# Kernel optimization log

Measured on AMD Instinct MI355X. Metric: run time of the kernel, lower is better.

Reference implementation:

```python
import jax, jax.numpy as jnp
import numpy as np

N_RAYS = 65536
N_SAMPLES = 96


def setup_inputs() -> dict:
    key = jax.random.key(0)
    k1, k2, k3 = jax.random.split(key, 3)
    rgb = jax.random.uniform(k1, (N_RAYS, N_SAMPLES, 3), dtype=jnp.float32)
    # SDF values near the surface, small magnitude
    sdf = jax.random.normal(k2, (N_RAYS, N_SAMPLES), dtype=jnp.float32) * 0.1
    # monotonically increasing sample depths along each ray
    z_vals = jnp.sort(
        jax.random.uniform(k3, (N_RAYS, N_SAMPLES), dtype=jnp.float32,
                           minval=0.1, maxval=5.0), axis=-1)
    return {"rgb": rgb, "sdf": sdf, "z_vals": z_vals, "beta": 10}


def reference(rgb, sdf, z_vals, beta):
    # sdf2alpha: alpha = 1 - exp(-beta * sigmoid(-sdf * beta))
    alpha = 1.0 - jnp.exp(-beta * jax.nn.sigmoid(-sdf * beta))  # [N, S]
    # exclusive cumprod of (1 - alpha + 1e-10): transmittance
    trans = jnp.cumprod(
        jnp.concatenate([jnp.ones_like(alpha[:, :1]), 1.0 - alpha + 1e-10],
                        axis=-1), axis=-1)[:, :-1]  # [N, S]
    weights = alpha * trans  # [N, S]
    rendered_rgb = jnp.sum(weights[..., None] * rgb, axis=-2)  # [N, 3]
    rendered_depth = jnp.sum(weights * z_vals, axis=-1)  # [N]
    return (rendered_depth, rendered_rgb, sdf, z_vals)
```

## Files before the change

### kernel.cpp

```cpp
#include <hip/hip_runtime.h>


#define SDFR_NS 96

struct f3 { float x, y, z; };
typedef float fv4 __attribute__((ext_vector_type(4)));

__global__ __launch_bounds__(256, 8) void sdf_compute_kernel(
    const float* __restrict__ rgb,
    const float* __restrict__ sdf,
    const float* __restrict__ z_vals,
    const int*   __restrict__ beta_p,
    float* __restrict__ out_depth,
    float* __restrict__ out_rgb,
    int n_rays)
{
    const int tid = blockIdx.x * 256 + threadIdx.x;
    const int ray = tid >> 5;
    const int l   = tid & 31;
    if (ray >= n_rays) return;

    const int sb = ray * SDFR_NS + 3 * l;
    const int rb = ray * (SDFR_NS * 3) + 9 * l;

    const f3 sv = *(const f3*)(sdf    + sb);
    const f3 zv = *(const f3*)(z_vals + sb);
    const f3 ca = *(const f3*)(rgb + rb + 0);
    const f3 cb = *(const f3*)(rgb + rb + 3);
    const f3 cc = *(const f3*)(rgb + rb + 6);
    __builtin_amdgcn_sched_barrier(0);

    int bi = *beta_p;
    float beta;
    if (bi > 1000000 || bi < -1000000) {
        union { int i; float f; } u; u.i = bi; beta = u.f;
    } else {
        beta = (float)bi;
    }

    const float e0 = __expf(-beta * __builtin_amdgcn_rcpf(1.0f + __expf(sv.x * beta)));
    const float e1 = __expf(-beta * __builtin_amdgcn_rcpf(1.0f + __expf(sv.y * beta)));
    const float e2 = __expf(-beta * __builtin_amdgcn_rcpf(1.0f + __expf(sv.z * beta)));
    const float a0 = 1.0f - e0, t0 = e0 + 1e-10f;
    const float a1 = 1.0f - e1, t1 = e1 + 1e-10f;
    const float a2 = 1.0f - e2, t2 = e2 + 1e-10f;

    float scan = t0 * t1 * t2;
    #pragma unroll
    for (int d = 1; d < 32; d <<= 1) {
        float v = __shfl_up(scan, d, 32);
        if (l >= d) scan *= v;
    }
    float E = __shfl_up(scan, 1, 32);
    if (l == 0) E = 1.0f;

    const float w0 = a0 * E;
    const float w1 = a1 * E * t0;
    const float w2 = a2 * E * t0 * t1;

    float depth = w0 * zv.x + w1 * zv.y + w2 * zv.z;
    float r0    = w0 * ca.x + w1 * cb.x + w2 * cc.x;
    float r1    = w0 * ca.y + w1 * cb.y + w2 * cc.y;
    float r2    = w0 * ca.z + w1 * cb.z + w2 * cc.z;

    #pragma unroll
    for (int d = 16; d >= 1; d >>= 1) {
        depth += __shfl_xor(depth, d, 32);
        r0    += __shfl_xor(r0, d, 32);
        r1    += __shfl_xor(r1, d, 32);
        r2    += __shfl_xor(r2, d, 32);
    }

    if (l == 0) {
        out_depth[ray] = depth;
        f3 o; o.x = r0; o.y = r1; o.z = r2;
        *(f3*)(out_rgb + ray * 3) = o;
    }
}

#define SDFR_CPB 2048

__global__ __launch_bounds__(256, 8) void sdf_copy_kernel(
    const float* __restrict__ sdf,
    const float* __restrict__ z_vals,
    float* __restrict__ out_sdf,
    float* __restrict__ out_z,
    int n_rays)
{
    const int n4     = (n_rays * SDFR_NS) / 4;
    const int stride = SDFR_CPB * 256;
    const fv4* __restrict__ s4 = (const fv4*)sdf;
    const fv4* __restrict__ z4 = (const fv4*)z_vals;
    fv4* __restrict__ os4 = (fv4*)out_sdf;
    fv4* __restrict__ oz4 = (fv4*)out_z;

    for (int i = blockIdx.x * 256 + threadIdx.x; i < n4; i += stride) {
        const fv4 a = s4[i];
        const fv4 b = z4[i];
        __builtin_nontemporal_store(a, os4 + i);
        __builtin_nontemporal_store(b, oz4 + i);
    }
}

extern "C" void kernel_launch(void* const* d_in, const int* in_sizes, int n_in,
                              void* d_out, int out_size, void* d_ws, size_t ws_size,
                              hipStream_t stream) {
    (void)n_in; (void)d_ws; (void)ws_size; (void)out_size;

    const float* rgb    = (const float*)d_in[0];
    const float* sdf    = (const float*)d_in[1];
    const float* z      = (const float*)d_in[2];
    const int*   beta_p = (const int*)d_in[3];

    const int n_rays = in_sizes[1] / SDFR_NS;

    float* out_depth = (float*)d_out;
    float* out_rgb   = out_depth + n_rays;
    float* out_sdf   = out_rgb   + (size_t)n_rays * 3;
    float* out_z     = out_sdf   + (size_t)n_rays * SDFR_NS;

    const int comp_blocks = (n_rays * 32 + 255) / 256;
    sdf_compute_kernel<<<comp_blocks, 256, 0, stream>>>(
        rgb, sdf, z, beta_p, out_depth, out_rgb, n_rays);

    sdf_copy_kernel<<<SDFR_CPB, 256, 0, stream>>>(
        sdf, z, out_sdf, out_z, n_rays);
}
```

Baseline: 175.1 us.

## Stage ray inputs into LDS via direct global-to-LDS loads with XCD-aware block remap

The compute kernel now loads each block's 8 rays of sdf, z and rgb into shared memory with 16-byte global_load_lds transfers instead of uncoalesced 12-byte per-lane vector loads. Lanes then read their three samples from LDS. Block indices are also remapped so that consecutive blocks land on the same XCD, which is meant to improve L2 locality. This adds a barrier and LDS traffic, and the remap assumes the grid size is divisible by 8.

```diff
diff --git a/kernel.cpp b/kernel.cpp
--- a/kernel.cpp
+++ b/kernel.cpp
@@ -2,9 +2,10 @@
 
 
 #define SDFR_NS 96
+#define SDFR_RPB 8
 
+typedef float fv4 __attribute__((ext_vector_type(4)));
 struct f3 { float x, y, z; };
-typedef float fv4 __attribute__((ext_vector_type(4)));
 
 __global__ __launch_bounds__(256, 8) void sdf_compute_kernel(
     const float* __restrict__ rgb,
@@ -15,20 +16,66 @@
     float* __restrict__ out_rgb,
     int n_rays)
 {
-    const int tid = blockIdx.x * 256 + threadIdx.x;
-    const int ray = tid >> 5;
-    const int l   = tid & 31;
+    __shared__ __align__(16) float lds[SDFR_RPB * SDFR_NS * 5];
+
+    const int t = threadIdx.x;
+
+    const int cpx = (int)(gridDim.x >> 3);
+    const int blk = (int)((blockIdx.x & 7) * cpx + (blockIdx.x >> 3));
+
+    const int base_ray = blk * SDFR_RPB;
+    const int g   = t >> 5;
+    const int l   = t & 31;
+    const int ray = base_ray + g;
+
+    const bool full = (base_ray + SDFR_RPB <= n_rays);
+
+    if (full) {
+        const int lane = t & 63;
+        const int w    = t >> 6;
+        char* lb = (char*)lds;
+        #pragma unroll
+        for (int k = 0; k < 4; ++k) {
+            const int s = w + k * 4;
+            if (s < 15) {
+                const char* src;
+                if (s < 3)
+                    src = (const char*)sdf    + (size_t)blk * 3072 + (size_t)s * 1024;
+                else if (s < 6)
+                    src = (const char*)z_vals + (size_t)blk * 3072 + (size_t)(s - 3) * 1024;
+                else
+                    src = (const char*)rgb    + (size_t)blk * 9216 + (size_t)(s - 6) * 1024;
+                __builtin_amdgcn_global_load_lds(
+                    (const __attribute__((address_space(1))) void*)(src + lane * 16),
+                    (__attribute__((address_space(3))) void*)(lb + s * 1024),
+                    16, 0, 0);
+            }
+        }
+    } else {
+        const int flim = n_rays * SDFR_NS;
+        for (int i = t; i < SDFR_RPB * SDFR_NS; i += 256) {
+            const int gi = base_ray * SDFR_NS + i;
+            lds[i]       = (gi < flim) ? sdf[gi]    : 0.f;
+            lds[768 + i] = (gi < flim) ? z_vals[gi] : 0.f;
+        }
+        const int clim = n_rays * SDFR_NS * 3;
+        for (int i = t; i < SDFR_RPB * SDFR_NS * 3; i += 256) {
+            const int gi = base_ray * SDFR_NS * 3 + i;
+            lds[1536 + i] = (gi < clim) ? rgb[gi] : 0.f;
+        }
+    }
+
+    __syncthreads();
     if (ray >= n_rays) return;
 
-    const int sb = ray * SDFR_NS + 3 * l;
-    const int rb = ray * (SDFR_NS * 3) + 9 * l;
-
-    const f3 sv = *(const f3*)(sdf    + sb);
-    const f3 zv = *(const f3*)(z_vals + sb);
-    const f3 ca = *(const f3*)(rgb + rb + 0);
-    const f3 cb = *(const f3*)(rgb + rb + 3);
-    const f3 cc = *(const f3*)(rgb + rb + 6);
-    __builtin_amdgcn_sched_barrier(0);
+    const float* sf = lds + g * SDFR_NS + 3 * l;
+    const float* zf = lds + 768 + g * SDFR_NS + 3 * l;
+    const float* cf = lds + 1536 + g * (SDFR_NS * 3) + 9 * l;
+    const float s0 = sf[0], s1 = sf[1], s2 = sf[2];
+    const float z0 = zf[0], z1 = zf[1], z2 = zf[2];
+    const float c0 = cf[0], c1 = cf[1], c2 = cf[2];
+    const float c3 = cf[3], c4 = cf[4], c5 = cf[5];
+    const float c6 = cf[6], c7 = cf[7], c8 = cf[8];
 
     int bi = *beta_p;
     float beta;
@@ -38,9 +85,9 @@
         beta = (float)bi;
     }
 
-    const float e0 = __expf(-beta * __builtin_amdgcn_rcpf(1.0f + __expf(sv.x * beta)));
-    const float e1 = __expf(-beta * __builtin_amdgcn_rcpf(1.0f + __expf(sv.y * beta)));
-    const float e2 = __expf(-beta * __builtin_amdgcn_rcpf(1.0f + __expf(sv.z * beta)));
+    const float e0 = __expf(-beta * __builtin_amdgcn_rcpf(1.0f + __expf(s0 * beta)));
+    const float e1 = __expf(-beta * __builtin_amdgcn_rcpf(1.0f + __expf(s1 * beta)));
+    const float e2 = __expf(-beta * __builtin_amdgcn_rcpf(1.0f + __expf(s2 * beta)));
     const float a0 = 1.0f - e0, t0 = e0 + 1e-10f;
     const float a1 = 1.0f - e1, t1 = e1 + 1e-10f;
     const float a2 = 1.0f - e2, t2 = e2 + 1e-10f;
@@ -58,10 +105,10 @@
     const float w1 = a1 * E * t0;
     const float w2 = a2 * E * t0 * t1;
 
-    float depth = w0 * zv.x + w1 * zv.y + w2 * zv.z;
-    float r0    = w0 * ca.x + w1 * cb.x + w2 * cc.x;
-    float r1    = w0 * ca.y + w1 * cb.y + w2 * cc.y;
-    float r2    = w0 * ca.z + w1 * cb.z + w2 * cc.z;
+    float depth = w0 * z0 + w1 * z1 + w2 * z2;
+    float r0    = w0 * c0 + w1 * c3 + w2 * c6;
+    float r1    = w0 * c1 + w1 * c4 + w2 * c7;
+    float r2    = w0 * c2 + w1 * c5 + w2 * c8;
 
     #pragma unroll
     for (int d = 16; d >= 1; d >>= 1) {
@@ -119,7 +166,7 @@
     float* out_sdf   = out_rgb   + (size_t)n_rays * 3;
     float* out_z     = out_sdf   + (size_t)n_rays * SDFR_NS;
 
-    const int comp_blocks = (n_rays * 32 + 255) / 256;
+    const int comp_blocks = (n_rays + SDFR_RPB - 1) / SDFR_RPB;
     sdf_compute_kernel<<<comp_blocks, 256, 0, stream>>>(
         rgb, sdf, z, beta_p, out_depth, out_rgb, n_rays);
 
```

After: 177.3 us. No clear change (+1.2%).
